# Kernel tuning notes

Measured on AMD Instinct MI355X. Metric: run time of the kernel, lower is better.

Reference implementation:

```python
import jax, jax.numpy as jnp
import numpy as np

B, N, C, H, W = 4, 8, 256, 64, 64
SCALE = 2
D = C * SCALE  # embed_dim*scale, head_size with n_heads=1
EPS = 1e-6


def setup_inputs() -> dict:
    key = jax.random.key(0)
    ks = jax.random.split(key, 6)
    sc = lambda k, sh, f: jax.random.normal(k, sh, jnp.float32) * f
    return {
        "q": jax.random.normal(ks[0], (B, C), jnp.float32),
        "c": jax.random.normal(ks[1], (B, N, C, H, W), jnp.float32),
        "g": jnp.ones((C,), jnp.float32),                 # RMSNorm weight
        "Wq": sc(ks[2], (D, C), C ** -0.5),               # proj_q weight
        "Wkv": sc(ks[3], (2 * D, C), C ** -0.5),          # proj_kv weight
        "Wo": sc(ks[4], (C, D), D ** -0.5),               # proj_out weight
        "bo": jnp.zeros((C,), jnp.float32),               # proj_out bias
    }


def reference(q, c, g, Wq, Wkv, Wo, bo):
    # c: [B,N,C,H,W] -> [B,H,W,N,C]
    cp = jnp.transpose(c, (0, 3, 4, 1, 2))
    # RMSNorm over channel dim
    cn = cp * jax.lax.rsqrt(jnp.mean(cp * cp, axis=-1, keepdims=True) + EPS) * g
    # per-pixel, per-token k/v projection: [B,H,W,N,2D]
    kv = jnp.einsum('bhwnc,dc->bhwnd', cn, Wkv)
    k, v = jnp.split(kv, 2, axis=-1)                      # each [B,H,W,N,D]
    qp = q @ Wq.T                                         # [B,D]
    # broadcast single query over spatial grid; softmax over N context tokens
    dots = jnp.einsum('bd,bhwnd->bhwn', qp, k) * (D ** -0.5)
    att = jax.nn.softmax(dots, axis=-1)                   # [B,H,W,N]
    hvec = jnp.einsum('bhwn,bhwnd->bhwd', att, v)         # [B,H,W,D]
    out = hvec @ Wo.T + bo                                # [B,H,W,C]
    return jnp.transpose(out, (0, 3, 1, 2))               # [B,C,H,W]
```

## Files before the change

### kernel.cpp

```cpp
#include <hip/hip_runtime.h>


typedef __attribute__((ext_vector_type(8))) short short8;
typedef __attribute__((ext_vector_type(4))) float floatx4;

static __device__ __forceinline__ short f2bf(float f) {
  unsigned u = __float_as_uint(f);
  u += 0x7fffu + ((u >> 16) & 1u);
  return (short)(u >> 16);
}

__global__ __launch_bounds__(256) void pre_kernel(
    const float* __restrict__ q, const float* __restrict__ g,
    const float* __restrict__ Wq, const float* __restrict__ Wkv,
    const float* __restrict__ Wo, unsigned char* __restrict__ ws) {
  short* WovgB = (short*)ws;
  float* gqk = (float*)(ws + 131072);
  const int blk = blockIdx.x, tid = threadIdx.x;
  if (blk < 256) {
    const int i = blk, c = tid;
    float s = 0.f;
    #pragma unroll 8
    for (int d = 0; d < 512; ++d)
      s = fmaf(Wo[i * 512 + d], Wkv[(512 + d) * 256 + c], s);
    WovgB[i * 256 + c] = f2bf(s * g[c]);
  } else {
    const int b = blk - 256;
    __shared__ float qps[512];
    for (int d = tid; d < 512; d += 256) {
      float s = 0.f;
      #pragma unroll 8
      for (int cc = 0; cc < 256; ++cc)
        s = fmaf(Wq[d * 256 + cc], q[b * 256 + cc], s);
      qps[d] = s;
    }
    __syncthreads();
    const int c = tid;
    float s = 0.f;
    #pragma unroll 8
    for (int d = 0; d < 512; ++d)
      s = fmaf(Wkv[d * 256 + c], qps[d], s);
    gqk[b * 256 + c] = s * g[c] * 0.044194173824159216f;
  }
}

__global__ __launch_bounds__(512) void attn_kernel(
    const float* __restrict__ cin, const float* __restrict__ bo,
    const unsigned char* __restrict__ ws, float* __restrict__ out) {
  const short* WovgB = (const short*)ws;
  const float* gqk = (const float*)(ws + 131072);
  const int blk = blockIdx.x;
  const int b = blk >> 6, h = blk & 63;
  const int tid = threadIdx.x;
  const int lane = tid & 63;
  const int cg = tid >> 6;

  __shared__ short tB[8][4][64][8];
  __shared__ float red_ssq[8][64];
  __shared__ float red_dot[8][64];
  __shared__ float m_s[64], z_s[64], al_s[64], wn_s[64];

  float rg[32];
  #pragma unroll
  for (int j = 0; j < 32; ++j) rg[j] = gqk[b * 256 + cg * 32 + j];

  if (tid < 64) { m_s[tid] = -1e30f; z_s[tid] = 0.f; }
  float t_reg[32];
  #pragma unroll
  for (int j = 0; j < 32; ++j) t_reg[j] = 0.f;
  __syncthreads();

  const float* cb = cin + ((size_t)(b * 8) * 256 + cg * 32) * 4096 + h * 64 + lane;
  for (int n = 0; n < 8; ++n) {
    const float* cp = cb + (size_t)n * 256 * 4096;
    float vals[32];
    #pragma unroll
    for (int j = 0; j < 32; ++j) vals[j] = cp[(size_t)j * 4096];
    float ssq = 0.f, dt = 0.f;
    #pragma unroll
    for (int j = 0; j < 32; ++j) {
      ssq = fmaf(vals[j], vals[j], ssq);
      dt = fmaf(vals[j], rg[j], dt);
    }
    red_ssq[cg][lane] = ssq;
    red_dot[cg][lane] = dt;
    __syncthreads();
    if (tid < 64) {
      float S = 0.f, Dt = 0.f;
      #pragma unroll
      for (int gg = 0; gg < 8; ++gg) { S += red_ssq[gg][tid]; Dt += red_dot[gg][tid]; }
      const float invr = rsqrtf(S * (1.f / 256.f) + 1e-6f);
      const float d = Dt * invr;
      const float mo = m_s[tid];
      const float mn = fmaxf(mo, d);
      const float al = __expf(mo - mn);
      const float e = __expf(d - mn);
      z_s[tid] = z_s[tid] * al + e;
      m_s[tid] = mn;
      al_s[tid] = al;
      wn_s[tid] = e * invr;
    }
    __syncthreads();
    const float al = al_s[lane], wn = wn_s[lane];
    #pragma unroll
    for (int j = 0; j < 32; ++j) t_reg[j] = fmaf(wn, vals[j], t_reg[j] * al);
  }

  {
    const float invZ = 1.f / z_s[lane];
    const int nt = lane >> 4, m = lane & 15;
    #pragma unroll
    for (int qq = 0; qq < 4; ++qq) {
      short8 pk;
      #pragma unroll
      for (int jj = 0; jj < 8; ++jj) pk[jj] = f2bf(t_reg[qq * 8 + jj] * invZ);
      *(short8*)(&tB[cg][nt][qq * 16 + m][0]) = pk;
    }
  }
  __syncthreads();

  const int ig = __builtin_amdgcn_readfirstlane(tid >> 6);
  const int q = lane >> 4, m = lane & 15;
  const short8* Av = (const short8*)WovgB;
  const short8* Bv = (const short8*)tB;
  floatx4 acc[2][4];
  #pragma unroll
  for (int mt = 0; mt < 2; ++mt)
    #pragma unroll
    for (int nt = 0; nt < 4; ++nt) acc[mt][nt] = (floatx4){0.f, 0.f, 0.f, 0.f};
  #pragma unroll
  for (int s = 0; s < 8; ++s) {
    const short8 a0 = Av[(ig * 32 + m) * 32 + s * 4 + q];
    const short8 a1 = Av[(ig * 32 + 16 + m) * 32 + s * 4 + q];
    #pragma unroll
    for (int nt = 0; nt < 4; ++nt) {
      const short8 bf = Bv[(s * 4 + nt) * 64 + lane];
      acc[0][nt] = __builtin_amdgcn_mfma_f32_16x16x32_bf16(a0, bf, acc[0][nt], 0, 0, 0);
      acc[1][nt] = __builtin_amdgcn_mfma_f32_16x16x32_bf16(a1, bf, acc[1][nt], 0, 0, 0);
    }
  }
  float bov[2][4];
  #pragma unroll
  for (int mt = 0; mt < 2; ++mt)
    #pragma unroll
    for (int r = 0; r < 4; ++r) bov[mt][r] = bo[ig * 32 + mt * 16 + q * 4 + r];
  float* ob = out + ((size_t)b * 256) * 4096 + h * 64;
  #pragma unroll
  for (int mt = 0; mt < 2; ++mt)
    #pragma unroll
    for (int nt = 0; nt < 4; ++nt)
      #pragma unroll
      for (int r = 0; r < 4; ++r) {
        const int i = ig * 32 + mt * 16 + q * 4 + r;
        const int px = nt * 16 + m;
        ob[(size_t)i * 4096 + px] = acc[mt][nt][r] + bov[mt][r];
      }
}

extern "C" void kernel_launch(void* const* d_in, const int* in_sizes, int n_in,
                              void* d_out, int out_size, void* d_ws, size_t ws_size,
                              hipStream_t stream) {
  const float* q   = (const float*)d_in[0];
  const float* c   = (const float*)d_in[1];
  const float* g   = (const float*)d_in[2];
  const float* Wq  = (const float*)d_in[3];
  const float* Wkv = (const float*)d_in[4];
  const float* Wo  = (const float*)d_in[5];
  const float* bo  = (const float*)d_in[6];
  float* out = (float*)d_out;
  unsigned char* ws = (unsigned char*)d_ws;
  pre_kernel<<<260, 256, 0, stream>>>(q, g, Wq, Wkv, Wo, ws);
  attn_kernel<<<256, 512, 0, stream>>>(c, bo, ws, out);
}
```

Baseline: 268.6 us.

## Split attention blocks to half-rows and replace shared-memory softmax with shuffles

The attention kernel now runs 512 blocks of 256 threads, each handling 32 pixels of a row. Channel groups are split across wave halves and reduced with a cross-lane shuffle plus a double-buffered shared array, so the separate single-wave softmax step and one barrier per token go away. Every thread keeps its own running max and denominator in registers. The precomputed Wo·Wv weight is stored in an MFMA-fragment-friendly tiled layout so A-fragment loads are contiguous. The loop unroll factors in the pre-kernel also change. In exchange each thread repeats the softmax math, and each block fetches a larger share of the weight tile.

```diff
diff --git a/kernel.cpp b/kernel.cpp
--- a/kernel.cpp
+++ b/kernel.cpp
@@ -20,16 +20,18 @@
   if (blk < 256) {
     const int i = blk, c = tid;
     float s = 0.f;
-    #pragma unroll 8
+    #pragma unroll 16
     for (int d = 0; d < 512; ++d)
       s = fmaf(Wo[i * 512 + d], Wkv[(512 + d) * 256 + c], s);
-    WovgB[i * 256 + c] = f2bf(s * g[c]);
+    const int it = i >> 4, m = i & 15;
+    const int sg = c >> 5, q2 = (c >> 3) & 3, jj = c & 7;
+    WovgB[((((it * 8 + sg) * 4 + q2) * 16) + m) * 8 + jj] = f2bf(s * g[c]);
   } else {
     const int b = blk - 256;
     __shared__ float qps[512];
     for (int d = tid; d < 512; d += 256) {
       float s = 0.f;
-      #pragma unroll 8
+      #pragma unroll 16
       for (int cc = 0; cc < 256; ++cc)
         s = fmaf(Wq[d * 256 + cc], q[b * 256 + cc], s);
       qps[d] = s;
@@ -37,40 +39,39 @@
     __syncthreads();
     const int c = tid;
     float s = 0.f;
-    #pragma unroll 8
+    #pragma unroll 16
     for (int d = 0; d < 512; ++d)
       s = fmaf(Wkv[d * 256 + c], qps[d], s);
     gqk[b * 256 + c] = s * g[c] * 0.044194173824159216f;
   }
 }
 
-__global__ __launch_bounds__(512) void attn_kernel(
+__global__ __launch_bounds__(256, 2) void attn_kernel(
     const float* __restrict__ cin, const float* __restrict__ bo,
     const unsigned char* __restrict__ ws, float* __restrict__ out) {
-  const short* WovgB = (const short*)ws;
+  const short8* Av = (const short8*)ws;
   const float* gqk = (const float*)(ws + 131072);
   const int blk = blockIdx.x;
-  const int b = blk >> 6, h = blk & 63;
+  const int b = blk >> 7, h = (blk >> 1) & 63, hf = blk & 1;
   const int tid = threadIdx.x;
-  const int lane = tid & 63;
-  const int cg = tid >> 6;
+  const int lane = tid & 63, w = tid >> 6;
+  const int px = lane & 31, cgh = lane >> 5;
+  const int cg = w * 2 + cgh;
 
-  __shared__ short tB[8][4][64][8];
-  __shared__ float red_ssq[8][64];
-  __shared__ float red_dot[8][64];
-  __shared__ float m_s[64], z_s[64], al_s[64], wn_s[64];
+  __shared__ short tB[8][2][64][8];
+  __shared__ float redS[2][4][32], redD[2][4][32];
 
   float rg[32];
   #pragma unroll
   for (int j = 0; j < 32; ++j) rg[j] = gqk[b * 256 + cg * 32 + j];
 
-  if (tid < 64) { m_s[tid] = -1e30f; z_s[tid] = 0.f; }
   float t_reg[32];
   #pragma unroll
   for (int j = 0; j < 32; ++j) t_reg[j] = 0.f;
-  __syncthreads();
+  float mM = -1e30f, zZ = 0.f;
 
-  const float* cb = cin + ((size_t)(b * 8) * 256 + cg * 32) * 4096 + h * 64 + lane;
+  const float* cb = cin + ((size_t)(b * 8) * 256 + cg * 32) * 4096
+                        + h * 64 + hf * 32 + px;
   for (int n = 0; n < 8; ++n) {
     const float* cp = cb + (size_t)n * 256 * 4096;
     float vals[32];
@@ -82,79 +83,74 @@
       ssq = fmaf(vals[j], vals[j], ssq);
       dt = fmaf(vals[j], rg[j], dt);
     }
-    red_ssq[cg][lane] = ssq;
-    red_dot[cg][lane] = dt;
+    ssq += __shfl_xor(ssq, 32);
+    dt  += __shfl_xor(dt, 32);
+    if (cgh == 0) { redS[n & 1][w][px] = ssq; redD[n & 1][w][px] = dt; }
     __syncthreads();
-    if (tid < 64) {
-      float S = 0.f, Dt = 0.f;
-      #pragma unroll
-      for (int gg = 0; gg < 8; ++gg) { S += red_ssq[gg][tid]; Dt += red_dot[gg][tid]; }
-      const float invr = rsqrtf(S * (1.f / 256.f) + 1e-6f);
-      const float d = Dt * invr;
-      const float mo = m_s[tid];
-      const float mn = fmaxf(mo, d);
-      const float al = __expf(mo - mn);
-      const float e = __expf(d - mn);
-      z_s[tid] = z_s[tid] * al + e;
-      m_s[tid] = mn;
-      al_s[tid] = al;
-      wn_s[tid] = e * invr;
-    }
-    __syncthreads();
-    const float al = al_s[lane], wn = wn_s[lane];
+    float S = 0.f, Dt = 0.f;
+    #pragma unroll
+    for (int ww = 0; ww < 4; ++ww) { S += redS[n & 1][ww][px]; Dt += redD[n & 1][ww][px]; }
+    const float invr = rsqrtf(S * (1.f / 256.f) + 1e-6f);
+    const float d = Dt * invr;
+    const float mn = fmaxf(mM, d);
+    const float al = __expf(mM - mn);
+    const float e = __expf(d - mn);
+    zZ = zZ * al + e;
+    mM = mn;
+    const float wn = e * invr;
     #pragma unroll
     for (int j = 0; j < 32; ++j) t_reg[j] = fmaf(wn, vals[j], t_reg[j] * al);
   }
 
   {
-    const float invZ = 1.f / z_s[lane];
-    const int nt = lane >> 4, m = lane & 15;
+    const float invZ = 1.f / zZ;
+    const int nt = px >> 4, mm = px & 15;
     #pragma unroll
     for (int qq = 0; qq < 4; ++qq) {
       short8 pk;
       #pragma unroll
       for (int jj = 0; jj < 8; ++jj) pk[jj] = f2bf(t_reg[qq * 8 + jj] * invZ);
-      *(short8*)(&tB[cg][nt][qq * 16 + m][0]) = pk;
+      *(short8*)(&tB[cg][nt][qq * 16 + mm][0]) = pk;
     }
   }
   __syncthreads();
 
-  const int ig = __builtin_amdgcn_readfirstlane(tid >> 6);
+  const int ig = __builtin_amdgcn_readfirstlane(w);
   const int q = lane >> 4, m = lane & 15;
-  const short8* Av = (const short8*)WovgB;
   const short8* Bv = (const short8*)tB;
-  floatx4 acc[2][4];
+  floatx4 acc[4][2];
   #pragma unroll
-  for (int mt = 0; mt < 2; ++mt)
+  for (int mt = 0; mt < 4; ++mt)
     #pragma unroll
-    for (int nt = 0; nt < 4; ++nt) acc[mt][nt] = (floatx4){0.f, 0.f, 0.f, 0.f};
+    for (int nt = 0; nt < 2; ++nt) acc[mt][nt] = (floatx4){0.f, 0.f, 0.f, 0.f};
   #pragma unroll
   for (int s = 0; s < 8; ++s) {
-    const short8 a0 = Av[(ig * 32 + m) * 32 + s * 4 + q];
-    const short8 a1 = Av[(ig * 32 + 16 + m) * 32 + s * 4 + q];
+    short8 a[4];
     #pragma unroll
-    for (int nt = 0; nt < 4; ++nt) {
-      const short8 bf = Bv[(s * 4 + nt) * 64 + lane];
-      acc[0][nt] = __builtin_amdgcn_mfma_f32_16x16x32_bf16(a0, bf, acc[0][nt], 0, 0, 0);
-      acc[1][nt] = __builtin_amdgcn_mfma_f32_16x16x32_bf16(a1, bf, acc[1][nt], 0, 0, 0);
+    for (int mt = 0; mt < 4; ++mt)
+      a[mt] = Av[(((ig * 4 + mt) * 8 + s) * 4 + q) * 16 + m];
+    #pragma unroll
+    for (int nt = 0; nt < 2; ++nt) {
+      const short8 bf = Bv[(s * 2 + nt) * 64 + lane];
+      #pragma unroll
+      for (int mt = 0; mt < 4; ++mt)
+        acc[mt][nt] = __builtin_amdgcn_mfma_f32_16x16x32_bf16(a[mt], bf, acc[mt][nt], 0, 0, 0);
     }
   }
-  float bov[2][4];
+  float* ob = out + (size_t)b * 256 * 4096 + h * 64 + hf * 32;
   #pragma unroll
-  for (int mt = 0; mt < 2; ++mt)
+  for (int mt = 0; mt < 4; ++mt) {
+    float bov[4];
     #pragma unroll
-    for (int r = 0; r < 4; ++r) bov[mt][r] = bo[ig * 32 + mt * 16 + q * 4 + r];
-  float* ob = out + ((size_t)b * 256) * 4096 + h * 64;
-  #pragma unroll
-  for (int mt = 0; mt < 2; ++mt)
+    for (int r = 0; r < 4; ++r) bov[r] = bo[ig * 64 + mt * 16 + q * 4 + r];
     #pragma unroll
-    for (int nt = 0; nt < 4; ++nt)
+    for (int nt = 0; nt < 2; ++nt)
       #pragma unroll
       for (int r = 0; r < 4; ++r) {
-        const int i = ig * 32 + mt * 16 + q * 4 + r;
-        const int px = nt * 16 + m;
-        ob[(size_t)i * 4096 + px] = acc[mt][nt][r] + bov[mt][r];
+        const int i = ig * 64 + mt * 16 + q * 4 + r;
+        ob[(size_t)i * 4096 + nt * 16 + m] = acc[mt][nt][r] + bov[r];
       }
+  }
 }
 
 extern "C" void kernel_launch(void* const* d_in, const int* in_sizes, int n_in,
@@ -170,5 +166,5 @@
   float* out = (float*)d_out;
   unsigned char* ws = (unsigned char*)d_ws;
   pre_kernel<<<260, 256, 0, stream>>>(q, g, Wq, Wkv, Wo, ws);
-  attn_kernel<<<256, 512, 0, stream>>>(c, bo, ws, out);
+  attn_kernel<<<512, 256, 0, stream>>>(c, bo, ws, out);
 }
```

After: 249.4 us. 7.1% less time.
